# Kernel tuning notes

Hardware: AMD Instinct MI355X
Metric: run time of the kernel (lower is better)

## Reference

```python
import jax, jax.numpy as jnp
import numpy as np

N_C = 100000   # customer nodes
N_P = 100000   # product_order nodes
E = 1600000    # edges per relation
D_IN = 64
D_H = 32
D_OUT = 1


def setup_inputs() -> dict:
    key = jax.random.key(0)
    ks = jax.random.split(key, 20)
    s = lambda d: 1.0 / np.sqrt(d)
    inp = {
        "x_customer": jax.random.normal(ks[0], (N_C, D_IN), jnp.float32),
        "x_product": jax.random.normal(ks[1], (N_P, D_IN), jnp.float32),
        "edge_c2p": jax.random.randint(ks[2], (2, E), 0, N_C, jnp.int32),  # row0 src(customer), row1 dst(product)
        "edge_p2c": jax.random.randint(ks[3], (2, E), 0, N_P, jnp.int32),  # row0 src(product), row1 dst(customer)
        # conv1, relation customer->product_order
        "W1l_r1": jax.random.normal(ks[4], (D_IN, D_H), jnp.float32) * s(D_IN),
        "b1_r1": jnp.zeros((D_H,), jnp.float32),
        "W1r_r1": jax.random.normal(ks[5], (D_IN, D_H), jnp.float32) * s(D_IN),
        # conv1, relation product_order->customer
        "W1l_r2": jax.random.normal(ks[6], (D_IN, D_H), jnp.float32) * s(D_IN),
        "b1_r2": jnp.zeros((D_H,), jnp.float32),
        "W1r_r2": jax.random.normal(ks[7], (D_IN, D_H), jnp.float32) * s(D_IN),
        # conv2, relation customer->product_order
        "W2l_r1": jax.random.normal(ks[8], (D_H, D_H), jnp.float32) * s(D_H),
        "b2_r1": jnp.zeros((D_H,), jnp.float32),
        "W2r_r1": jax.random.normal(ks[9], (D_H, D_H), jnp.float32) * s(D_H),
        # conv2, relation product_order->customer
        "W2l_r2": jax.random.normal(ks[10], (D_H, D_H), jnp.float32) * s(D_H),
        "b2_r2": jnp.zeros((D_H,), jnp.float32),
        "W2r_r2": jax.random.normal(ks[11], (D_H, D_H), jnp.float32) * s(D_H),
        # final per-node-type linear (only product_order output is used)
        "Wlin": jax.random.normal(ks[12], (D_H, D_OUT), jnp.float32) * s(D_H),
        "blin": jnp.zeros((D_OUT,), jnp.float32),
    }
    return inp


def _sage(x_src, x_dst, edge, Wl, bl, Wr, n_dst):
    # SAGEConv with mean aggregation: lin_l(mean_{j in N(i)} x_j) + lin_r(x_i)
    src, dst = edge[0], edge[1]
    msg = x_src[src]                                   # [E, d] gather
    agg = jax.ops.segment_sum(msg, dst, num_segments=n_dst)
    cnt = jax.ops.segment_sum(jnp.ones((edge.shape[1],), x_src.dtype), dst,
                              num_segments=n_dst)
    mean = agg / jnp.maximum(cnt, 1.0)[:, None]
    return mean @ Wl + bl + x_dst @ Wr


def reference(x_customer, x_product, edge_c2p, edge_p2c,
              W1l_r1, b1_r1, W1r_r1, W1l_r2, b1_r2, W1r_r2,
              W2l_r1, b2_r1, W2r_r1, W2l_r2, b2_r2, W2r_r2,
              Wlin, blin):
    # layer 1 (to_hetero aggr='sum'; each dst type has exactly one incoming relation)
    h_p = jax.nn.relu(_sage(x_customer, x_product, edge_c2p,
                            W1l_r1, b1_r1, W1r_r1, N_P))
    h_c = jax.nn.relu(_sage(x_product, x_customer, edge_p2c,
                            W1l_r2, b1_r2, W1r_r2, N_C))
    # layer 2
    h_p2 = _sage(h_c, h_p, edge_c2p, W2l_r1, b2_r1, W2r_r1, N_P)
    # output head on product_order nodes
    logits = h_p2 @ Wlin + blin
    return jax.nn.sigmoid(logits)
```

## Files before the change

### kernel.cpp

```cpp
#include <hip/hip_runtime.h>
#include <stdint.h>

#define BB 9
#define BSZ 512
#define STAGE_CAP 12288

__global__ void fill_zero_i4(int4* __restrict__ p, size_t n4) {
    size_t i = (size_t)blockIdx.x * blockDim.x + threadIdx.x;
    size_t stride = (size_t)gridDim.x * blockDim.x;
    for (; i < n4; i += stride) p[i] = make_int4(0, 0, 0, 0);
}

__global__ void khist(const int* __restrict__ e1, const int* __restrict__ e2, int E,
                      int* __restrict__ gcnt1, int* __restrict__ gcnt2,
                      int nb1, int nb2, int blocksPerRel) {
    int rel = blockIdx.x >= blocksPerRel;
    int blk = rel ? blockIdx.x - blocksPerRel : blockIdx.x;
    const int* dst = (rel ? e2 : e1) + E;
    int* gcnt = rel ? gcnt2 : gcnt1;
    int nb = rel ? nb2 : nb1;
    __shared__ int cnt[256];
    for (int i = threadIdx.x; i < 256; i += 256) cnt[i] = 0;
    __syncthreads();
    int base = blk * 8192;
#pragma unroll
    for (int k = 0; k < 32; k++) {
        int i = base + k * 256 + threadIdx.x;
        if (i < E) atomicAdd(&cnt[dst[i] >> BB], 1);
    }
    __syncthreads();
    for (int b = threadIdx.x; b < nb; b += 256)
        if (cnt[b]) atomicAdd(&gcnt[b], cnt[b]);
}

__global__ void kscan(const int* __restrict__ gcnt1, int* __restrict__ boff1,
                      int* __restrict__ gcur1, int nb1,
                      const int* __restrict__ gcnt2, int* __restrict__ boff2,
                      int* __restrict__ gcur2, int nb2, int E) {
    const int* gcnt = blockIdx.x ? gcnt2 : gcnt1;
    int* boff = blockIdx.x ? boff2 : boff1;
    int* gcur = blockIdx.x ? gcur2 : gcur1;
    int nb = blockIdx.x ? nb2 : nb1;
    __shared__ int wsum[4];
    int tid = threadIdx.x, lane = tid & 63, wid = tid >> 6;
    int v = (tid < nb) ? gcnt[tid] : 0;
    int sc = v;
#pragma unroll
    for (int off = 1; off < 64; off <<= 1) {
        int t = __shfl_up(sc, off, 64);
        if (lane >= off) sc += t;
    }
    if (lane == 63) wsum[wid] = sc;
    __syncthreads();
    int woff = 0;
    for (int w = 0; w < wid; w++) woff += wsum[w];
    int excl = woff + sc - v;
    if (tid < nb) { boff[tid] = excl; gcur[tid] = excl; }
    if (tid == nb - 1) boff[nb] = excl + v;
}

__global__ void kbin(const int* __restrict__ e1, const int* __restrict__ e2, int E,
                     int* __restrict__ gcur1, int* __restrict__ gcur2,
                     unsigned int* __restrict__ P1, unsigned int* __restrict__ P2,
                     int blocksPerRel) {
    int rel = blockIdx.x >= blocksPerRel;
    int blk = rel ? blockIdx.x - blocksPerRel : blockIdx.x;
    const int* edge = rel ? e2 : e1;
    int* gcur = rel ? gcur2 : gcur1;
    unsigned int* P = rel ? P2 : P1;
    __shared__ int cnt[256];
    __shared__ int base[256];
    for (int i = threadIdx.x; i < 256; i += 256) cnt[i] = 0;
    __syncthreads();
    int cbase = blk * 4096;
    int src[16], dst[16], rk[16];
#pragma unroll
    for (int k = 0; k < 16; k++) {
        int i = cbase + k * 256 + threadIdx.x;
        if (i < E) {
            src[k] = edge[i];
            dst[k] = edge[E + i];
            rk[k] = atomicAdd(&cnt[dst[k] >> BB], 1);
        }
    }
    __syncthreads();
    for (int b = threadIdx.x; b < 256; b += 256)
        base[b] = cnt[b] ? atomicAdd(&gcur[b], cnt[b]) : 0;
    __syncthreads();
#pragma unroll
    for (int k = 0; k < 16; k++) {
        int i = cbase + k * 256 + threadIdx.x;
        if (i < E) {
            int b = dst[k] >> BB;
            P[base[b] + rk[k]] =
                ((unsigned)src[k] << BB) | (unsigned)(dst[k] & (BSZ - 1));
        }
    }
}

__global__ void kbsort(const unsigned int* __restrict__ P1, const unsigned int* __restrict__ P2,
                       const int* __restrict__ boff1, const int* __restrict__ boff2,
                       int* __restrict__ ss1, int* __restrict__ ss2,
                       int* __restrict__ ro1, int* __restrict__ ro2,
                       int n1, int n2, int nb1, int nb2, int E) {
    int rel = blockIdx.x >= nb1;
    int b = rel ? blockIdx.x - nb1 : blockIdx.x;
    const unsigned int* P = rel ? P2 : P1;
    const int* boff = rel ? boff2 : boff1;
    int* ss = rel ? ss2 : ss1;
    int* ro = rel ? ro2 : ro1;
    int N = rel ? n2 : n1;
    int nb = rel ? nb2 : nb1;

    __shared__ int cnt[BSZ];
    __shared__ int cur[BSZ];
    __shared__ int wsum[8];
    __shared__ int stage[STAGE_CAP];

    int s = boff[b], e = boff[b + 1];
    int m = e - s;
    int d0 = b << BB;
    int nd = min(BSZ, N - d0);
    int tid = threadIdx.x;

    cnt[tid] = 0;
    __syncthreads();
    for (int i = tid; i < m; i += 512) atomicAdd(&cnt[P[s + i] & (BSZ - 1)], 1);
    __syncthreads();
    int lane = tid & 63, wid = tid >> 6;
    int v = cnt[tid], sc = v;
#pragma unroll
    for (int off = 1; off < 64; off <<= 1) {
        int t = __shfl_up(sc, off, 64);
        if (lane >= off) sc += t;
    }
    if (lane == 63) wsum[wid] = sc;
    __syncthreads();
    int woff = 0;
    for (int w = 0; w < wid; w++) woff += wsum[w];
    int excl = woff + sc - v;
    cur[tid] = excl;
    if (tid < nd) ro[d0 + tid] = s + excl;
    if (tid == 0 && b == nb - 1) ro[N] = E;
    __syncthreads();
    for (int i = tid; i < m; i += 512) {
        unsigned int p = P[s + i];
        int slot = atomicAdd(&cur[p & (BSZ - 1)], 1);
        if (slot < STAGE_CAP) stage[slot] = (int)(p >> BB);
    }
    __syncthreads();
    for (int i = tid; i < m; i += 512) ss[s + i] = stage[i];
}

__global__ void head_pre(const float* __restrict__ W2l, const float* __restrict__ W2r,
                         const float* __restrict__ b2, const float* __restrict__ Wlin,
                         const float* __restrict__ blin, float* __restrict__ hconst) {
    int t = threadIdx.x;
    if (t < 64) {
        const float* W = (t < 32) ? W2l : W2r;
        int k = t & 31;
        float acc = 0.0f;
#pragma unroll
        for (int j = 0; j < 32; j++) acc += W[k * 32 + j] * Wlin[j];
        hconst[t] = acc;
    }
    if (t == 64) {
        float acc = blin[0];
#pragma unroll
        for (int j = 0; j < 32; j++) acc += b2[j] * Wlin[j];
        hconst[64] = acc;
    }
}

__global__ void proj_tile(
    const float* __restrict__ x1, const float* __restrict__ Wy1, const float* __restrict__ Ws1,
    _Float16* __restrict__ y1, float* __restrict__ s1, int N1, int blocks1,
    const float* __restrict__ x2, const float* __restrict__ Wy2, const float* __restrict__ Ws2,
    _Float16* __restrict__ y2, float* __restrict__ s2, int N2) {
    int rel = blockIdx.x >= blocks1;
    int blk = rel ? blockIdx.x - blocks1 : blockIdx.x;
    const float* x = rel ? x2 : x1;
    const float* Wy = rel ? Wy2 : Wy1;
    const float* Ws = rel ? Ws2 : Ws1;
    _Float16* y = rel ? y2 : y1;
    float* s = rel ? s2 : s1;
    int N = rel ? N2 : N1;

    __shared__ float xs[64][68];
    __shared__ float wyl[64][32];
    __shared__ float wsl[64][32];

    int tid = threadIdx.x;
    {
        const float4* a = (const float4*)Wy;
        const float4* b = (const float4*)Ws;
        float4* la = (float4*)&wyl[0][0];
        float4* lb = (float4*)&wsl[0][0];
        la[tid] = a[tid];
        la[tid + 256] = a[tid + 256];
        lb[tid] = b[tid];
        lb[tid + 256] = b[tid + 256];
    }
    int base = blk << 6;
#pragma unroll
    for (int i = 0; i < 4; i++) {
        int idx = i * 256 + tid;
        int row = idx >> 4, c4 = (idx & 15) << 2;
        int node = base + row;
        float4 v = (node < N) ? *(const float4*)(x + ((size_t)node << 6) + c4)
                              : make_float4(0.f, 0.f, 0.f, 0.f);
        *(float4*)&xs[row][c4] = v;
    }
    __syncthreads();

    int node = tid & 63;
    int ob = (tid >> 6) << 3;
    float ay[8] = {0,0,0,0,0,0,0,0};
    float as_[8] = {0,0,0,0,0,0,0,0};
#pragma unroll
    for (int kc = 0; kc < 16; kc++) {
        float4 xv = *(float4*)&xs[node][kc << 2];
#pragma unroll
        for (int kk = 0; kk < 4; kk++) {
            int k = (kc << 2) + kk;
            float xk = (kk == 0) ? xv.x : (kk == 1) ? xv.y : (kk == 2) ? xv.z : xv.w;
            float4 a = *(float4*)&wyl[k][ob];
            float4 b = *(float4*)&wyl[k][ob + 4];
            float4 c = *(float4*)&wsl[k][ob];
            float4 d = *(float4*)&wsl[k][ob + 4];
            ay[0] += xk * a.x; ay[1] += xk * a.y; ay[2] += xk * a.z; ay[3] += xk * a.w;
            ay[4] += xk * b.x; ay[5] += xk * b.y; ay[6] += xk * b.z; ay[7] += xk * b.w;
            as_[0] += xk * c.x; as_[1] += xk * c.y; as_[2] += xk * c.z; as_[3] += xk * c.w;
            as_[4] += xk * d.x; as_[5] += xk * d.y; as_[6] += xk * d.z; as_[7] += xk * d.w;
        }
    }
    int ng = base + node;
    if (ng < N) {
        union { _Float16 h[8]; uint4 v; } u;
#pragma unroll
        for (int j = 0; j < 8; j++) u.h[j] = (_Float16)ay[j];
        *(uint4*)(y + ((size_t)ng << 5) + ob) = u.v;
        *(float4*)(s + ((size_t)ng << 5) + ob) =
            make_float4(as_[0], as_[1], as_[2], as_[3]);
        *(float4*)(s + ((size_t)ng << 5) + ob + 4) =
            make_float4(as_[4], as_[5], as_[6], as_[7]);
    }
}

__global__ void pull_l1_both(
    const int* __restrict__ ro_p, const int* __restrict__ ssp, const _Float16* __restrict__ y_c,
    const float* __restrict__ sp, const float* __restrict__ b_p, const float* __restrict__ hconst,
    float* __restrict__ u_p, int NP, int blocksP,
    const int* __restrict__ ro_c, const int* __restrict__ ssc, const _Float16* __restrict__ y_p,
    const float* __restrict__ sc_, const float* __restrict__ b_c, float* __restrict__ t_c, int NC) {
    int rel = blockIdx.x >= blocksP;
    int blk = rel ? blockIdx.x - blocksP : blockIdx.x;
    const int* ro = rel ? ro_c : ro_p;
    const int* ss = rel ? ssc : ssp;
    const _Float16* y = rel ? y_p : y_c;
    const float* sf = rel ? sc_ : sp;
    const float* bv = rel ? b_c : b_p;
    const float* v2 = rel ? hconst : hconst + 32;
    float* tgt = rel ? t_c : u_p;
    int N = rel ? NC : NP;

    int gid = blk * 256 + threadIdx.x;
    int node = gid >> 5, od = gid & 31;
    if (node >= N) return;
    int start = ro[node], end = ro[node + 1];
    float acc = 0.0f;
    int j = start;
    for (; j + 3 < end; j += 4) {
        int a0 = ss[j], a1 = ss[j + 1], a2 = ss[j + 2], a3 = ss[j + 3];
        acc += (float)y[((size_t)a0 << 5) + od] + (float)y[((size_t)a1 << 5) + od]
             + (float)y[((size_t)a2 << 5) + od] + (float)y[((size_t)a3 << 5) + od];
    }
    for (; j < end; j++) acc += (float)y[((size_t)ss[j] << 5) + od];
    float r = bv[od] + sf[((size_t)node << 5) + od]
            + acc / fmaxf((float)(end - start), 1.0f);
    float p = fmaxf(r, 0.0f) * v2[od];
#pragma unroll
    for (int off = 16; off > 0; off >>= 1) p += __shfl_xor(p, off, 32);
    if (od == 0) tgt[node] = p;
}

__global__ void pull_l2_scalar(const int* __restrict__ ro, const int* __restrict__ ss,
                               const float* __restrict__ t_c, const float* __restrict__ u_p,
                               const float* __restrict__ hconst,
                               float* __restrict__ out, int N) {
    int gid = blockIdx.x * blockDim.x + threadIdx.x;
    int node = gid >> 2, ln = gid & 3;
    if (node >= N) return;
    int s = ro[node], e = ro[node + 1];
    float acc = 0.0f;
    for (int j = s + ln; j < e; j += 4) acc += t_c[ss[j]];
    acc += __shfl_xor(acc, 1, 4);
    acc += __shfl_xor(acc, 2, 4);
    if (ln == 0) {
        float logit = acc / fmaxf((float)(e - s), 1.0f) + u_p[node] + hconst[64];
        out[node] = 1.0f / (1.0f + expf(-logit));
    }
}

extern "C" void kernel_launch(void* const* d_in, const int* in_sizes, int n_in,
                              void* d_out, int out_size, void* d_ws, size_t ws_size,
                              hipStream_t stream) {
    const float* xc    = (const float*)d_in[0];
    const float* xp    = (const float*)d_in[1];
    const int*   e_c2p = (const int*)d_in[2];
    const int*   e_p2c = (const int*)d_in[3];
    const float* W1l_r1 = (const float*)d_in[4];
    const float* b1_r1  = (const float*)d_in[5];
    const float* W1r_r1 = (const float*)d_in[6];
    const float* W1l_r2 = (const float*)d_in[7];
    const float* b1_r2  = (const float*)d_in[8];
    const float* W1r_r2 = (const float*)d_in[9];
    const float* W2l_r1 = (const float*)d_in[10];
    const float* b2_r1  = (const float*)d_in[11];
    const float* W2r_r1 = (const float*)d_in[12];
    const float* Wlin  = (const float*)d_in[16];
    const float* blin  = (const float*)d_in[17];
    float* out = (float*)d_out;

    const int NC = in_sizes[0] / 64;
    const int NP = in_sizes[1] / 64;
    const int E  = in_sizes[2] / 2;
    const int nbP = (NP + BSZ - 1) >> BB;
    const int nbC = (NC + BSZ - 1) >> BB;

    char* w = (char*)d_ws;
    int* gcnt_p = (int*)w;  w += 256 * 4;
    int* gcnt_c = (int*)w;  w += 256 * 4;
    int* gcur_p = (int*)w;  w += 256 * 4;
    int* gcur_c = (int*)w;  w += 256 * 4;
    int* boff_p = (int*)w;  w += 257 * 4;
    int* boff_c = (int*)w;  w += 257 * 4;
    float* hconst = (float*)w; w += 68 * 4;
    w = (char*)(((uintptr_t)w + 255) & ~(uintptr_t)255);
    size_t szPair = (size_t)E * 4;
    if ((size_t)NP * 64 > szPair) szPair = (size_t)NP * 64;
    if ((size_t)NC * 64 > szPair) szPair = (size_t)NC * 64;
    unsigned int* P_p = (unsigned int*)w;  w += szPair;
    unsigned int* P_c = (unsigned int*)w;  w += szPair;
    int* ss_p = (int*)w;    w += (size_t)E * 4;
    int* ss_c = (int*)w;    w += (size_t)E * 4;
    int* ro_p = (int*)w;    w += (size_t)(NP + 1) * 4;
    int* ro_c = (int*)w;    w += (size_t)(NC + 1) * 4;
    w = (char*)(((uintptr_t)w + 255) & ~(uintptr_t)255);
    float* s_p = (float*)w; w += (size_t)NP * 32 * 4;
    float* s_c = (float*)w; w += (size_t)NC * 32 * 4;
    float* t_c = (float*)w; w += (size_t)NC * 4;
    float* u_p = (float*)w; w += (size_t)NP * 4;
    _Float16* y_c = (_Float16*)P_p;
    _Float16* y_p = (_Float16*)P_c;

    const int bprH = (E + 8191) / 8192;
    const int bprB = (E + 4095) / 4096;

    fill_zero_i4<<<1, 128, 0, stream>>>((int4*)gcnt_p, 128);
    head_pre<<<1, 128, 0, stream>>>(W2l_r1, W2r_r1, b2_r1, Wlin, blin, hconst);

    khist<<<2 * bprH, 256, 0, stream>>>(e_c2p, e_p2c, E, gcnt_p, gcnt_c, nbP, nbC, bprH);
    kscan<<<2, 256, 0, stream>>>(gcnt_p, boff_p, gcur_p, nbP, gcnt_c, boff_c, gcur_c, nbC, E);
    kbin<<<2 * bprB, 256, 0, stream>>>(e_c2p, e_p2c, E, gcur_p, gcur_c, P_p, P_c, bprB);
    kbsort<<<nbP + nbC, 512, 0, stream>>>(P_p, P_c, boff_p, boff_c,
                                          ss_p, ss_c, ro_p, ro_c, NP, NC, nbP, nbC, E);

    const int tblocksC = (NC + 63) / 64;
    const int tblocksP = (NP + 63) / 64;
    proj_tile<<<tblocksC + tblocksP, 256, 0, stream>>>(
        xc, W1l_r1, W1r_r2, y_c, s_c, NC, tblocksC,
        xp, W1l_r2, W1r_r1, y_p, s_p, NP);

    const int blocksP = (NP * 32 + 255) / 256;
    const int blocksC = (NC * 32 + 255) / 256;
    pull_l1_both<<<blocksP + blocksC, 256, 0, stream>>>(
        ro_p, ss_p, y_c, s_p, b1_r1, hconst, u_p, NP, blocksP,
        ro_c, ss_c, y_p, s_c, b1_r2, t_c, NC);

    pull_l2_scalar<<<(NP * 4 + 255) / 256, 256, 0, stream>>>(
        ro_p, ss_p, t_c, u_p, hconst, out, NP);
}
```

Baseline: 301.8 us.

## Replace per-node CSR sort with bucket-level shared-memory atomic aggregation

Drops the kbsort pass that built a full CSR (ro/ss arrays). Layer-1 and layer-2 aggregation now work directly on the destination-binned edge buckets, with each block accumulating sums and counts for its 512 destinations in shared memory through LDS float atomics. This removes a full sort kernel and the index indirection, and y gets its own buffer instead of aliasing P. The cost is heavy LDS atomic contention: 32 atomics per edge in layer 1. The per-node segmented reads in the pull kernels are replaced by a scatter pattern, and the float summation order is no longer deterministic.

```diff
diff --git a/kernel.cpp b/kernel.cpp
--- a/kernel.cpp
+++ b/kernel.cpp
@@ -3,7 +3,6 @@
 
 #define BB 9
 #define BSZ 512
-#define STAGE_CAP 12288
 
 __global__ void fill_zero_i4(int4* __restrict__ p, size_t n4) {
     size_t i = (size_t)blockIdx.x * blockDim.x + threadIdx.x;
@@ -96,60 +95,6 @@
                 ((unsigned)src[k] << BB) | (unsigned)(dst[k] & (BSZ - 1));
         }
     }
-}
-
-__global__ void kbsort(const unsigned int* __restrict__ P1, const unsigned int* __restrict__ P2,
-                       const int* __restrict__ boff1, const int* __restrict__ boff2,
-                       int* __restrict__ ss1, int* __restrict__ ss2,
-                       int* __restrict__ ro1, int* __restrict__ ro2,
-                       int n1, int n2, int nb1, int nb2, int E) {
-    int rel = blockIdx.x >= nb1;
-    int b = rel ? blockIdx.x - nb1 : blockIdx.x;
-    const unsigned int* P = rel ? P2 : P1;
-    const int* boff = rel ? boff2 : boff1;
-    int* ss = rel ? ss2 : ss1;
-    int* ro = rel ? ro2 : ro1;
-    int N = rel ? n2 : n1;
-    int nb = rel ? nb2 : nb1;
-
-    __shared__ int cnt[BSZ];
-    __shared__ int cur[BSZ];
-    __shared__ int wsum[8];
-    __shared__ int stage[STAGE_CAP];
-
-    int s = boff[b], e = boff[b + 1];
-    int m = e - s;
-    int d0 = b << BB;
-    int nd = min(BSZ, N - d0);
-    int tid = threadIdx.x;
-
-    cnt[tid] = 0;
-    __syncthreads();
-    for (int i = tid; i < m; i += 512) atomicAdd(&cnt[P[s + i] & (BSZ - 1)], 1);
-    __syncthreads();
-    int lane = tid & 63, wid = tid >> 6;
-    int v = cnt[tid], sc = v;
-#pragma unroll
-    for (int off = 1; off < 64; off <<= 1) {
-        int t = __shfl_up(sc, off, 64);
-        if (lane >= off) sc += t;
-    }
-    if (lane == 63) wsum[wid] = sc;
-    __syncthreads();
-    int woff = 0;
-    for (int w = 0; w < wid; w++) woff += wsum[w];
-    int excl = woff + sc - v;
-    cur[tid] = excl;
-    if (tid < nd) ro[d0 + tid] = s + excl;
-    if (tid == 0 && b == nb - 1) ro[N] = E;
-    __syncthreads();
-    for (int i = tid; i < m; i += 512) {
-        unsigned int p = P[s + i];
-        int slot = atomicAdd(&cur[p & (BSZ - 1)], 1);
-        if (slot < STAGE_CAP) stage[slot] = (int)(p >> BB);
-    }
-    __syncthreads();
-    for (int i = tid; i < m; i += 512) ss[s + i] = stage[i];
 }
 
 __global__ void head_pre(const float* __restrict__ W2l, const float* __restrict__ W2r,
@@ -247,58 +192,108 @@
     }
 }
 
-__global__ void pull_l1_both(
-    const int* __restrict__ ro_p, const int* __restrict__ ssp, const _Float16* __restrict__ y_c,
-    const float* __restrict__ sp, const float* __restrict__ b_p, const float* __restrict__ hconst,
-    float* __restrict__ u_p, int NP, int blocksP,
-    const int* __restrict__ ro_c, const int* __restrict__ ssc, const _Float16* __restrict__ y_p,
-    const float* __restrict__ sc_, const float* __restrict__ b_c, float* __restrict__ t_c, int NC) {
-    int rel = blockIdx.x >= blocksP;
-    int blk = rel ? blockIdx.x - blocksP : blockIdx.x;
-    const int* ro = rel ? ro_c : ro_p;
-    const int* ss = rel ? ssc : ssp;
-    const _Float16* y = rel ? y_p : y_c;
-    const float* sf = rel ? sc_ : sp;
-    const float* bv = rel ? b_c : b_p;
+__global__ void kbpull(
+    const unsigned int* __restrict__ P1, const unsigned int* __restrict__ P2,
+    const int* __restrict__ boff1, const int* __restrict__ boff2,
+    const _Float16* __restrict__ y1, const _Float16* __restrict__ y2,
+    const float* __restrict__ s1, const float* __restrict__ s2,
+    const float* __restrict__ bv1, const float* __restrict__ bv2,
+    const float* __restrict__ hconst,
+    float* __restrict__ u_p, float* __restrict__ t_c,
+    int nb1, int N1, int N2) {
+    int rel = blockIdx.x >= nb1;
+    int b = rel ? blockIdx.x - nb1 : blockIdx.x;
+    const unsigned int* P = rel ? P2 : P1;
+    const int* boff = rel ? boff2 : boff1;
+    const _Float16* y = rel ? y2 : y1;
+    const float* sf = rel ? s2 : s1;
+    const float* bv = rel ? bv2 : bv1;
     const float* v2 = rel ? hconst : hconst + 32;
     float* tgt = rel ? t_c : u_p;
-    int N = rel ? NC : NP;
-
-    int gid = blk * 256 + threadIdx.x;
-    int node = gid >> 5, od = gid & 31;
-    if (node >= N) return;
-    int start = ro[node], end = ro[node + 1];
-    float acc = 0.0f;
-    int j = start;
-    for (; j + 3 < end; j += 4) {
-        int a0 = ss[j], a1 = ss[j + 1], a2 = ss[j + 2], a3 = ss[j + 3];
-        acc += (float)y[((size_t)a0 << 5) + od] + (float)y[((size_t)a1 << 5) + od]
-             + (float)y[((size_t)a2 << 5) + od] + (float)y[((size_t)a3 << 5) + od];
-    }
-    for (; j < end; j++) acc += (float)y[((size_t)ss[j] << 5) + od];
-    float r = bv[od] + sf[((size_t)node << 5) + od]
-            + acc / fmaxf((float)(end - start), 1.0f);
-    float p = fmaxf(r, 0.0f) * v2[od];
-#pragma unroll
-    for (int off = 16; off > 0; off >>= 1) p += __shfl_xor(p, off, 32);
-    if (od == 0) tgt[node] = p;
-}
-
-__global__ void pull_l2_scalar(const int* __restrict__ ro, const int* __restrict__ ss,
-                               const float* __restrict__ t_c, const float* __restrict__ u_p,
-                               const float* __restrict__ hconst,
-                               float* __restrict__ out, int N) {
-    int gid = blockIdx.x * blockDim.x + threadIdx.x;
-    int node = gid >> 2, ln = gid & 3;
-    if (node >= N) return;
-    int s = ro[node], e = ro[node + 1];
-    float acc = 0.0f;
-    for (int j = s + ln; j < e; j += 4) acc += t_c[ss[j]];
-    acc += __shfl_xor(acc, 1, 4);
-    acc += __shfl_xor(acc, 2, 4);
-    if (ln == 0) {
-        float logit = acc / fmaxf((float)(e - s), 1.0f) + u_p[node] + hconst[64];
-        out[node] = 1.0f / (1.0f + expf(-logit));
+    int N = rel ? N2 : N1;
+
+    __shared__ __align__(16) float acc[BSZ][33];
+    __shared__ int cnt[BSZ];
+
+    int tid = threadIdx.x;
+    {
+        float4* az = (float4*)&acc[0][0];
+        for (int i = tid; i < 4224; i += 256) az[i] = make_float4(0.f, 0.f, 0.f, 0.f);
+        for (int i = tid; i < BSZ; i += 256) cnt[i] = 0;
+    }
+    __syncthreads();
+
+    int s0 = boff[b], e0 = boff[b + 1];
+    int m = e0 - s0;
+    int sub = tid & 3;
+    int eo = tid >> 2;
+    for (int base = 0; base < m; base += 128) {
+        int i0 = base + eo, i1 = base + 64 + eo;
+        bool v0 = i0 < m, v1 = i1 < m;
+        unsigned p0 = v0 ? P[s0 + i0] : 0u;
+        unsigned p1 = v1 ? P[s0 + i1] : 0u;
+        uint4 q0, q1;
+        if (v0) q0 = *(const uint4*)(y + ((size_t)(p0 >> BB) << 5) + (sub << 3));
+        if (v1) q1 = *(const uint4*)(y + ((size_t)(p1 >> BB) << 5) + (sub << 3));
+        if (v0) {
+            int dl = p0 & (BSZ - 1);
+            union { uint4 v; _Float16 h[8]; } u; u.v = q0;
+#pragma unroll
+            for (int j = 0; j < 8; j++)
+                atomicAdd(&acc[dl][(sub << 3) + j], (float)u.h[j]);
+            if (sub == 0) atomicAdd(&cnt[dl], 1);
+        }
+        if (v1) {
+            int dl = p1 & (BSZ - 1);
+            union { uint4 v; _Float16 h[8]; } u; u.v = q1;
+#pragma unroll
+            for (int j = 0; j < 8; j++)
+                atomicAdd(&acc[dl][(sub << 3) + j], (float)u.h[j]);
+            if (sub == 0) atomicAdd(&cnt[dl], 1);
+        }
+    }
+    __syncthreads();
+
+    int d0 = b << BB;
+    int nd = min(BSZ, N - d0);
+    int od = tid & 31;
+    float vv = v2[od], bb = bv[od];
+    for (int n = tid >> 5; n < nd; n += 8) {
+        float a = acc[n][od];
+        float c = (float)cnt[n];
+        float r = bb + sf[((size_t)(d0 + n) << 5) + od] + a / fmaxf(c, 1.0f);
+        float pv = fmaxf(r, 0.0f) * vv;
+#pragma unroll
+        for (int off = 16; off > 0; off >>= 1) pv += __shfl_xor(pv, off, 32);
+        if (od == 0) tgt[d0 + n] = pv;
+    }
+}
+
+__global__ void kfin(const unsigned int* __restrict__ P, const int* __restrict__ boff,
+                     const float* __restrict__ t_c, const float* __restrict__ u_p,
+                     const float* __restrict__ hconst,
+                     float* __restrict__ out, int N) {
+    int b = blockIdx.x;
+    __shared__ float acc[BSZ];
+    __shared__ int cnt[BSZ];
+    int tid = threadIdx.x;
+    for (int i = tid; i < BSZ; i += 256) { acc[i] = 0.f; cnt[i] = 0; }
+    __syncthreads();
+    int s0 = boff[b], e0 = boff[b + 1], m = e0 - s0;
+    for (int i = tid; i < m; i += 256) {
+        unsigned p = P[s0 + i];
+        float v = t_c[p >> BB];
+        int dl = p & (BSZ - 1);
+        atomicAdd(&acc[dl], v);
+        atomicAdd(&cnt[dl], 1);
+    }
+    __syncthreads();
+    int d0 = b << BB;
+    int nd = min(BSZ, N - d0);
+    float cb = hconst[64];
+    for (int i = tid; i < nd; i += 256) {
+        float logit = acc[i] / fmaxf((float)cnt[i], 1.0f) + u_p[d0 + i] + cb;
+        out[d0 + i] = 1.0f / (1.0f + expf(-logit));
     }
 }
 
@@ -337,22 +332,16 @@
     int* boff_c = (int*)w;  w += 257 * 4;
     float* hconst = (float*)w; w += 68 * 4;
     w = (char*)(((uintptr_t)w + 255) & ~(uintptr_t)255);
-    size_t szPair = (size_t)E * 4;
-    if ((size_t)NP * 64 > szPair) szPair = (size_t)NP * 64;
-    if ((size_t)NC * 64 > szPair) szPair = (size_t)NC * 64;
-    unsigned int* P_p = (unsigned int*)w;  w += szPair;
-    unsigned int* P_c = (unsigned int*)w;  w += szPair;
-    int* ss_p = (int*)w;    w += (size_t)E * 4;
-    int* ss_c = (int*)w;    w += (size_t)E * 4;
-    int* ro_p = (int*)w;    w += (size_t)(NP + 1) * 4;
-    int* ro_c = (int*)w;    w += (size_t)(NC + 1) * 4;
+    unsigned int* P_p = (unsigned int*)w;  w += (size_t)E * 4;
+    unsigned int* P_c = (unsigned int*)w;  w += (size_t)E * 4;
+    w = (char*)(((uintptr_t)w + 255) & ~(uintptr_t)255);
+    _Float16* y_c = (_Float16*)w; w += (size_t)NC * 32 * 2;
+    _Float16* y_p = (_Float16*)w; w += (size_t)NP * 32 * 2;
     w = (char*)(((uintptr_t)w + 255) & ~(uintptr_t)255);
     float* s_p = (float*)w; w += (size_t)NP * 32 * 4;
     float* s_c = (float*)w; w += (size_t)NC * 32 * 4;
     float* t_c = (float*)w; w += (size_t)NC * 4;
     float* u_p = (float*)w; w += (size_t)NP * 4;
-    _Float16* y_c = (_Float16*)P_p;
-    _Float16* y_p = (_Float16*)P_c;
 
     const int bprH = (E + 8191) / 8192;
     const int bprB = (E + 4095) / 4096;
@@ -363,8 +352,6 @@
     khist<<<2 * bprH, 256, 0, stream>>>(e_c2p, e_p2c, E, gcnt_p, gcnt_c, nbP, nbC, bprH);
     kscan<<<2, 256, 0, stream>>>(gcnt_p, boff_p, gcur_p, nbP, gcnt_c, boff_c, gcur_c, nbC, E);
     kbin<<<2 * bprB, 256, 0, stream>>>(e_c2p, e_p2c, E, gcur_p, gcur_c, P_p, P_c, bprB);
-    kbsort<<<nbP + nbC, 512, 0, stream>>>(P_p, P_c, boff_p, boff_c,
-                                          ss_p, ss_c, ro_p, ro_c, NP, NC, nbP, nbC, E);
 
     const int tblocksC = (NC + 63) / 64;
     const int tblocksP = (NP + 63) / 64;
@@ -372,12 +359,9 @@
         xc, W1l_r1, W1r_r2, y_c, s_c, NC, tblocksC,
         xp, W1l_r2, W1r_r1, y_p, s_p, NP);
 
-    const int blocksP = (NP * 32 + 255) / 256;
-    const int blocksC = (NC * 32 + 255) / 256;
-    pull_l1_both<<<blocksP + blocksC, 256, 0, stream>>>(
-        ro_p, ss_p, y_c, s_p, b1_r1, hconst, u_p, NP, blocksP,
-        ro_c, ss_c, y_p, s_c, b1_r2, t_c, NC);
-
-    pull_l2_scalar<<<(NP * 4 + 255) / 256, 256, 0, stream>>>(
-        ro_p, ss_p, t_c, u_p, hconst, out, NP);
-}
+    kbpull<<<nbP + nbC, 256, 0, stream>>>(
+        P_p, P_c, boff_p, boff_c, y_c, y_p, s_p, s_c,
+        b1_r1, b1_r2, hconst, u_p, t_c, nbP, NP, NC);
+
+    kfin<<<nbP, 256, 0, stream>>>(P_p, boff_p, t_c, u_p, hconst, out, NP);
+}
```

Measured after the change: 922.7 us. 206% more time.
